# Optimization experiments

Measured on AMD Instinct MI355X. Metric: run time of the kernel, lower is better.

The kernel has to match this reference:

```python
import jax, jax.numpy as jnp
import numpy as np

NUM_RELS = 1000
NFEATS = 128
RFEATS = 64
B = 32768
P = 1  # norm order


def setup_inputs() -> dict:
    key = jax.random.key(0)
    k1, k2, k3, k4, k5 = jax.random.split(key, 5)
    h_head = jax.random.normal(k1, (B, NFEATS), dtype=jnp.float32)
    h_tail = jax.random.normal(k2, (B, NFEATS), dtype=jnp.float32)
    rels = jax.random.randint(k3, (B,), 0, NUM_RELS, dtype=jnp.int64)
    rel_emb_table = jax.random.normal(k4, (NUM_RELS, RFEATS), dtype=jnp.float32)
    rel_project_table = jax.random.normal(k5, (NUM_RELS, NFEATS * RFEATS), dtype=jnp.float32)
    return {
        "h_head": h_head,
        "h_tail": h_tail,
        "rels": rels,
        "rel_emb_table": rel_emb_table,
        "rel_project_table": rel_project_table,
    }


def reference(h_head, h_tail, rels, rel_emb_table, rel_project_table):
    # per-relation gathers
    h_rel = rel_emb_table[rels]                                    # [B, rfeats]
    proj_rel = rel_project_table[rels].reshape(-1, NFEATS, RFEATS)  # [B, nfeats, rfeats]
    # batched vector-matrix projection of head/tail into relation space
    ph = jnp.einsum("bn,bnr->br", h_head, proj_rel)               # [B, rfeats]
    pt = jnp.einsum("bn,bnr->br", h_tail, proj_rel)               # [B, rfeats]
    diff = ph + h_rel - pt                                         # [B, rfeats]
    # p=1 norm along last dim, negated score
    return -jnp.sum(jnp.abs(diff), axis=-1)                        # [B]
```

## Files before the change

### kernel.cpp

```cpp
#include <hip/hip_runtime.h>


#define NFEATS   128
#define RFEATS   64
#define NUM_RELS 1000
#define LIST_CAP 128

#define AS_GLOBAL __attribute__((address_space(1)))
#define AS_SHARED __attribute__((address_space(3)))

__global__ __launch_bounds__(512, 8) void transr_fused(
    const float* __restrict__ h_head,
    const float* __restrict__ h_tail,
    const int*   __restrict__ rels,
    const float* __restrict__ rel_emb,
    const float* __restrict__ rel_proj,
    float* __restrict__ out, int B)
{
    __shared__ float Plds[NFEATS * RFEATS];
    __shared__ int   list[LIST_CAP];
    __shared__ int   lcnt;

    const int r    = blockIdx.x;
    const int tid  = threadIdx.x;
    const int w    = tid >> 6;
    const int lane = tid & 63;

    if (tid == 0) lcnt = 0;
    __syncthreads();

    const float* Psrc = rel_proj + (size_t)r * (NFEATS * RFEATS);
#if __has_builtin(__builtin_amdgcn_global_load_lds)
#pragma unroll
    for (int it = 0; it < 4; ++it) {
        const int off = (it * 512 + tid) * 4;
        __builtin_amdgcn_global_load_lds(
            (const AS_GLOBAL void*)(Psrc + off),
            (AS_SHARED void*)(Plds + off), 16, 0, 0);
    }
#else
#pragma unroll
    for (int it = 0; it < 4; ++it) {
        const int off = (it * 512 + tid) * 4;
        *(float4*)(Plds + off) = *(const float4*)(Psrc + off);
    }
#endif

    {
        const int4* rels4 = (const int4*)rels;
        const int niter = B >> 11;
        for (int it = 0; it < niter; ++it) {
            const int idx  = it * 512 + tid;
            const int4 v   = rels4[idx];
            const int base = idx * 4;
            if (v.x == r) { int p = atomicAdd(&lcnt, 1); if (p < LIST_CAP) list[p] = base;     }
            if (v.y == r) { int p = atomicAdd(&lcnt, 1); if (p < LIST_CAP) list[p] = base + 1; }
            if (v.z == r) { int p = atomicAdd(&lcnt, 1); if (p < LIST_CAP) list[p] = base + 2; }
            if (v.w == r) { int p = atomicAdd(&lcnt, 1); if (p < LIST_CAP) list[p] = base + 3; }
        }
    }
    __syncthreads();

    int cnt = lcnt;
    if (cnt > LIST_CAP) cnt = LIST_CAP;

    const float ev = rel_emb[(size_t)r * RFEATS + lane];

    for (int base = 0; base < cnt; base += 32) {
        if (base + w * 4 >= cnt) break;

        int    rowid[4];
        float2 d2[4];
#pragma unroll
        for (int rr = 0; rr < 4; ++rr) {
            const int li = base + w * 4 + rr;
            rowid[rr] = (li < cnt) ? list[li] : -1;
            d2[rr] = make_float2(0.f, 0.f);
            if (rowid[rr] >= 0) {
                const float2 a = *(const float2*)(h_head + (size_t)rowid[rr] * NFEATS + lane * 2);
                const float2 b = *(const float2*)(h_tail + (size_t)rowid[rr] * NFEATS + lane * 2);
                d2[rr].x = a.x - b.x;
                d2[rr].y = a.y - b.y;
            }
        }

        float acc0 = 0.f, acc1 = 0.f, acc2 = 0.f, acc3 = 0.f;

#pragma unroll 8
        for (int q = 0; q < 64; ++q) {
            const float p0 = Plds[(2 * q) * RFEATS + lane];
            const float p1 = Plds[(2 * q + 1) * RFEATS + lane];

            float dx, dy;
            dx = __uint_as_float(__builtin_amdgcn_readlane(__float_as_uint(d2[0].x), q));
            dy = __uint_as_float(__builtin_amdgcn_readlane(__float_as_uint(d2[0].y), q));
            acc0 = fmaf(dx, p0, acc0); acc0 = fmaf(dy, p1, acc0);
            dx = __uint_as_float(__builtin_amdgcn_readlane(__float_as_uint(d2[1].x), q));
            dy = __uint_as_float(__builtin_amdgcn_readlane(__float_as_uint(d2[1].y), q));
            acc1 = fmaf(dx, p0, acc1); acc1 = fmaf(dy, p1, acc1);
            dx = __uint_as_float(__builtin_amdgcn_readlane(__float_as_uint(d2[2].x), q));
            dy = __uint_as_float(__builtin_amdgcn_readlane(__float_as_uint(d2[2].y), q));
            acc2 = fmaf(dx, p0, acc2); acc2 = fmaf(dy, p1, acc2);
            dx = __uint_as_float(__builtin_amdgcn_readlane(__float_as_uint(d2[3].x), q));
            dy = __uint_as_float(__builtin_amdgcn_readlane(__float_as_uint(d2[3].y), q));
            acc3 = fmaf(dx, p0, acc3); acc3 = fmaf(dy, p1, acc3);
        }

        float s[4] = { fabsf(acc0 + ev), fabsf(acc1 + ev),
                       fabsf(acc2 + ev), fabsf(acc3 + ev) };
#pragma unroll
        for (int rr = 0; rr < 4; ++rr) {
            float sv = s[rr];
            sv += __shfl_xor(sv, 1);
            sv += __shfl_xor(sv, 2);
            sv += __shfl_xor(sv, 4);
            sv += __shfl_xor(sv, 8);
            sv += __shfl_xor(sv, 16);
            sv += __shfl_xor(sv, 32);
            if (lane == rr && rowid[rr] >= 0) out[rowid[rr]] = -sv;
        }
    }
}

extern "C" void kernel_launch(void* const* d_in, const int* in_sizes, int n_in,
                              void* d_out, int out_size, void* d_ws, size_t ws_size,
                              hipStream_t stream) {
    const float* h_head   = (const float*)d_in[0];
    const float* h_tail   = (const float*)d_in[1];
    const int*   rels     = (const int*)d_in[2];
    const float* rel_emb  = (const float*)d_in[3];
    const float* rel_proj = (const float*)d_in[4];
    float* out = (float*)d_out;

    const int B = in_sizes[2];

    transr_fused<<<NUM_RELS, 512, 0, stream>>>(h_head, h_tail, rels, rel_emb,
                                               rel_proj, out, B);
}
```

Before: 131.2 us.

## Bucket rows by relation in a separate scatter kernel instead of per-block scans

Before, every one of the 1000 blocks scanned the whole rels array (32K entries) to collect the rows for its relation. A memset plus a global scatter kernel now builds per-relation buckets in workspace with atomics, and the main kernel reads its bucket directly. The first head/tail row loads are also issued before the barrier that waits for the projection tile to reach LDS, so they overlap it. The cost is two extra launches and global atomics, and the bucket order is nondeterministic.

```diff
diff --git a/kernel.cpp b/kernel.cpp
--- a/kernel.cpp
+++ b/kernel.cpp
@@ -4,30 +4,37 @@
 #define NFEATS   128
 #define RFEATS   64
 #define NUM_RELS 1000
-#define LIST_CAP 128
+#define STRIDE   128
 
 #define AS_GLOBAL __attribute__((address_space(1)))
 #define AS_SHARED __attribute__((address_space(3)))
 
-__global__ __launch_bounds__(512, 8) void transr_fused(
+__global__ void scatter_kernel(const int* __restrict__ rels,
+                               int* __restrict__ cursors,
+                               int* __restrict__ bucket, int B) {
+    int i = blockIdx.x * blockDim.x + threadIdx.x;
+    if (i < B) {
+        int r = rels[i];
+        int s = atomicAdd(&cursors[r], 1);
+        if (s < STRIDE) bucket[(r << 7) + s] = i;
+    }
+}
+
+__global__ __launch_bounds__(512, 8) void transr_main(
     const float* __restrict__ h_head,
     const float* __restrict__ h_tail,
-    const int*   __restrict__ rels,
     const float* __restrict__ rel_emb,
     const float* __restrict__ rel_proj,
-    float* __restrict__ out, int B)
+    const int*   __restrict__ cursors,
+    const int*   __restrict__ bucket,
+    float* __restrict__ out)
 {
     __shared__ float Plds[NFEATS * RFEATS];
-    __shared__ int   list[LIST_CAP];
-    __shared__ int   lcnt;
 
     const int r    = blockIdx.x;
     const int tid  = threadIdx.x;
     const int w    = tid >> 6;
     const int lane = tid & 63;
-
-    if (tid == 0) lcnt = 0;
-    __syncthreads();
 
     const float* Psrc = rel_proj + (size_t)r * (NFEATS * RFEATS);
 #if __has_builtin(__builtin_amdgcn_global_load_lds)
@@ -46,78 +53,82 @@
     }
 #endif
 
-    {
-        const int4* rels4 = (const int4*)rels;
-        const int niter = B >> 11;
-        for (int it = 0; it < niter; ++it) {
-            const int idx  = it * 512 + tid;
-            const int4 v   = rels4[idx];
-            const int base = idx * 4;
-            if (v.x == r) { int p = atomicAdd(&lcnt, 1); if (p < LIST_CAP) list[p] = base;     }
-            if (v.y == r) { int p = atomicAdd(&lcnt, 1); if (p < LIST_CAP) list[p] = base + 1; }
-            if (v.z == r) { int p = atomicAdd(&lcnt, 1); if (p < LIST_CAP) list[p] = base + 2; }
-            if (v.w == r) { int p = atomicAdd(&lcnt, 1); if (p < LIST_CAP) list[p] = base + 3; }
+    int cnt = cursors[r];
+    if (cnt > STRIDE) cnt = STRIDE;
+
+    const float ev = rel_emb[(size_t)r * RFEATS + lane];
+    const int* buk = bucket + (r << 7);
+
+    int    rowid[4];
+    float2 d2[4];
+#pragma unroll
+    for (int rr = 0; rr < 4; ++rr) {
+        const int li = w * 4 + rr;
+        rowid[rr] = (li < cnt) ? buk[li] : -1;
+        d2[rr] = make_float2(0.f, 0.f);
+        if (rowid[rr] >= 0) {
+            const float2 a = *(const float2*)(h_head + (size_t)rowid[rr] * NFEATS + lane * 2);
+            const float2 b = *(const float2*)(h_tail + (size_t)rowid[rr] * NFEATS + lane * 2);
+            d2[rr].x = a.x - b.x;
+            d2[rr].y = a.y - b.y;
         }
     }
+
     __syncthreads();
 
-    int cnt = lcnt;
-    if (cnt > LIST_CAP) cnt = LIST_CAP;
+    for (int base = 0; base < cnt; base += 32) {
+        if (base + w * 4 < cnt) {
+            float acc0 = 0.f, acc1 = 0.f, acc2 = 0.f, acc3 = 0.f;
 
-    const float ev = rel_emb[(size_t)r * RFEATS + lane];
+#pragma unroll 8
+            for (int q = 0; q < 64; ++q) {
+                const float p0 = Plds[(2 * q) * RFEATS + lane];
+                const float p1 = Plds[(2 * q + 1) * RFEATS + lane];
 
-    for (int base = 0; base < cnt; base += 32) {
-        if (base + w * 4 >= cnt) break;
+                float dx, dy;
+                dx = __uint_as_float(__builtin_amdgcn_readlane(__float_as_uint(d2[0].x), q));
+                dy = __uint_as_float(__builtin_amdgcn_readlane(__float_as_uint(d2[0].y), q));
+                acc0 = fmaf(dx, p0, acc0); acc0 = fmaf(dy, p1, acc0);
+                dx = __uint_as_float(__builtin_amdgcn_readlane(__float_as_uint(d2[1].x), q));
+                dy = __uint_as_float(__builtin_amdgcn_readlane(__float_as_uint(d2[1].y), q));
+                acc1 = fmaf(dx, p0, acc1); acc1 = fmaf(dy, p1, acc1);
+                dx = __uint_as_float(__builtin_amdgcn_readlane(__float_as_uint(d2[2].x), q));
+                dy = __uint_as_float(__builtin_amdgcn_readlane(__float_as_uint(d2[2].y), q));
+                acc2 = fmaf(dx, p0, acc2); acc2 = fmaf(dy, p1, acc2);
+                dx = __uint_as_float(__builtin_amdgcn_readlane(__float_as_uint(d2[3].x), q));
+                dy = __uint_as_float(__builtin_amdgcn_readlane(__float_as_uint(d2[3].y), q));
+                acc3 = fmaf(dx, p0, acc3); acc3 = fmaf(dy, p1, acc3);
+            }
 
-        int    rowid[4];
-        float2 d2[4];
+            float s[4] = { fabsf(acc0 + ev), fabsf(acc1 + ev),
+                           fabsf(acc2 + ev), fabsf(acc3 + ev) };
 #pragma unroll
-        for (int rr = 0; rr < 4; ++rr) {
-            const int li = base + w * 4 + rr;
-            rowid[rr] = (li < cnt) ? list[li] : -1;
-            d2[rr] = make_float2(0.f, 0.f);
-            if (rowid[rr] >= 0) {
-                const float2 a = *(const float2*)(h_head + (size_t)rowid[rr] * NFEATS + lane * 2);
-                const float2 b = *(const float2*)(h_tail + (size_t)rowid[rr] * NFEATS + lane * 2);
-                d2[rr].x = a.x - b.x;
-                d2[rr].y = a.y - b.y;
+            for (int rr = 0; rr < 4; ++rr) {
+                float sv = s[rr];
+                sv += __shfl_xor(sv, 1);
+                sv += __shfl_xor(sv, 2);
+                sv += __shfl_xor(sv, 4);
+                sv += __shfl_xor(sv, 8);
+                sv += __shfl_xor(sv, 16);
+                sv += __shfl_xor(sv, 32);
+                if (lane == rr && rowid[rr] >= 0) out[rowid[rr]] = -sv;
             }
         }
 
-        float acc0 = 0.f, acc1 = 0.f, acc2 = 0.f, acc3 = 0.f;
-
-#pragma unroll 8
-        for (int q = 0; q < 64; ++q) {
-            const float p0 = Plds[(2 * q) * RFEATS + lane];
-            const float p1 = Plds[(2 * q + 1) * RFEATS + lane];
-
-            float dx, dy;
-            dx = __uint_as_float(__builtin_amdgcn_readlane(__float_as_uint(d2[0].x), q));
-            dy = __uint_as_float(__builtin_amdgcn_readlane(__float_as_uint(d2[0].y), q));
-            acc0 = fmaf(dx, p0, acc0); acc0 = fmaf(dy, p1, acc0);
-            dx = __uint_as_float(__builtin_amdgcn_readlane(__float_as_uint(d2[1].x), q));
-            dy = __uint_as_float(__builtin_amdgcn_readlane(__float_as_uint(d2[1].y), q));
-            acc1 = fmaf(dx, p0, acc1); acc1 = fmaf(dy, p1, acc1);
-            dx = __uint_as_float(__builtin_amdgcn_readlane(__float_as_uint(d2[2].x), q));
-            dy = __uint_as_float(__builtin_amdgcn_readlane(__float_as_uint(d2[2].y), q));
-            acc2 = fmaf(dx, p0, acc2); acc2 = fmaf(dy, p1, acc2);
-            dx = __uint_as_float(__builtin_amdgcn_readlane(__float_as_uint(d2[3].x), q));
-            dy = __uint_as_float(__builtin_amdgcn_readlane(__float_as_uint(d2[3].y), q));
-            acc3 = fmaf(dx, p0, acc3); acc3 = fmaf(dy, p1, acc3);
-        }
-
-        float s[4] = { fabsf(acc0 + ev), fabsf(acc1 + ev),
-                       fabsf(acc2 + ev), fabsf(acc3 + ev) };
+        const int nbase = base + 32;
+        if (nbase < cnt) {
 #pragma unroll
-        for (int rr = 0; rr < 4; ++rr) {
-            float sv = s[rr];
-            sv += __shfl_xor(sv, 1);
-            sv += __shfl_xor(sv, 2);
-            sv += __shfl_xor(sv, 4);
-            sv += __shfl_xor(sv, 8);
-            sv += __shfl_xor(sv, 16);
-            sv += __shfl_xor(sv, 32);
-            if (lane == rr && rowid[rr] >= 0) out[rowid[rr]] = -sv;
+            for (int rr = 0; rr < 4; ++rr) {
+                const int li = nbase + w * 4 + rr;
+                rowid[rr] = (li < cnt) ? buk[li] : -1;
+                d2[rr] = make_float2(0.f, 0.f);
+                if (rowid[rr] >= 0) {
+                    const float2 a = *(const float2*)(h_head + (size_t)rowid[rr] * NFEATS + lane * 2);
+                    const float2 b = *(const float2*)(h_tail + (size_t)rowid[rr] * NFEATS + lane * 2);
+                    d2[rr].x = a.x - b.x;
+                    d2[rr].y = a.y - b.y;
+                }
+            }
         }
     }
 }
@@ -134,6 +145,11 @@
 
     const int B = in_sizes[2];
 
-    transr_fused<<<NUM_RELS, 512, 0, stream>>>(h_head, h_tail, rels, rel_emb,
-                                               rel_proj, out, B);
+    int* cursors = (int*)d_ws;
+    int* bucket  = cursors + 1024;
+
+    hipMemsetAsync(cursors, 0, 1024 * sizeof(int), stream);
+    scatter_kernel<<<(B + 255) / 256, 256, 0, stream>>>(rels, cursors, bucket, B);
+    transr_main<<<NUM_RELS, 512, 0, stream>>>(h_head, h_tail, rel_emb, rel_proj,
+                                              cursors, bucket, out);
 }
```

Result: slower. 134.9 us (+2.8%).
